# Kernel tuning notes

Hardware: AMD Instinct MI355X
Metric: run time of the kernel (lower is better)

Reference implementation:

```python
import jax, jax.numpy as jnp
import numpy as np

NB_HEAD = 16
SIZE_PER_HEAD = 64
D_MODEL = NB_HEAD * SIZE_PER_HEAD  # 1024
B, L = 2, 2048
NEG_BIG = 1e12


def setup_inputs() -> dict:
    key = jax.random.key(0)
    ks = jax.random.split(key, 8)
    return {
        "Q_seq": jax.random.normal(ks[0], (B, L, D_MODEL), dtype=jnp.float32),
        "K_seq": jax.random.normal(ks[1], (B, L, D_MODEL), dtype=jnp.float32),
        "V_seq": jax.random.normal(ks[2], (B, L, D_MODEL), dtype=jnp.float32),
        "q_len": jax.random.randint(ks[3], (B, 1), 1, L, dtype=jnp.int32),
        "v_len": jax.random.randint(ks[4], (B, 1), 1, L, dtype=jnp.int32),
        "WQ": jax.random.normal(ks[5], (D_MODEL, D_MODEL), dtype=jnp.float32) * 0.02,
        "WK": jax.random.normal(ks[6], (D_MODEL, D_MODEL), dtype=jnp.float32) * 0.02,
        "WV": jax.random.normal(ks[7], (D_MODEL, D_MODEL), dtype=jnp.float32) * 0.02,
    }


def _len_mask(lens, length, dtype):
    # Keras code: mask = 1 - cumsum(one_hot(len, L)) -> 1 for pos < len, 0 otherwise
    return (jnp.arange(length)[None, :] < lens).astype(dtype)  # [B, L]


def reference(Q_seq, K_seq, V_seq, q_len, v_len, WQ, WK, WV):
    Bq, Lq, _ = Q_seq.shape
    Lk = K_seq.shape[1]
    # QKV projections, split heads: [B, H, L, D]
    q = (Q_seq @ WQ).reshape(Bq, Lq, NB_HEAD, SIZE_PER_HEAD).transpose(0, 2, 1, 3)
    k = (K_seq @ WK).reshape(Bq, Lk, NB_HEAD, SIZE_PER_HEAD).transpose(0, 2, 1, 3)
    v = (V_seq @ WV).reshape(Bq, Lk, NB_HEAD, SIZE_PER_HEAD).transpose(0, 2, 1, 3)
    # scaled dot-product scores [B, H, Lq, Lk]
    scores = jnp.einsum("bhqd,bhkd->bhqk", q, k) / np.float32(SIZE_PER_HEAD ** 0.5)
    # additive key-length mask (V_len), matching Mask(..., 'add')
    kmask = _len_mask(v_len, Lk, scores.dtype)  # [B, Lk]
    scores = scores - (1.0 - kmask)[:, None, None, :] * np.float32(NEG_BIG)
    A = jax.nn.softmax(scores, axis=-1)
    # attention output, merge heads: [B, Lq, H*D]
    O = jnp.einsum("bhqk,bhkd->bqhd", A, v).reshape(Bq, Lq, D_MODEL)
    # multiplicative query-length mask (Q_len), matching Mask(..., 'mul')
    qmask = _len_mask(q_len, Lq, O.dtype)  # [B, Lq]
    return O * qmask[:, :, None]
```

## Files before the change

kernel.cpp:

```cpp
#include <hip/hip_runtime.h>
#include <cstddef>

#define NB_HEAD 16
#define HEAD_DIM 64
#define D_MODEL 1024
#define BATCH 2
#define SEQ 2048
#define MROWS (BATCH * SEQ)
#define NSPLIT 2

typedef __bf16 bf16x8 __attribute__((ext_vector_type(8)));
typedef __bf16 bf16x4 __attribute__((ext_vector_type(4)));
typedef float  f32x4  __attribute__((ext_vector_type(4)));

#define XEL ((size_t)MROWS * D_MODEL)
#define WEL ((size_t)D_MODEL * D_MODEL)

static __device__ __forceinline__ size_t xchunk(int row, int k) {
    return ((size_t)(row >> 4) * 32 + (k >> 5)) * 512 + ((k >> 3) & 3) * 128 + (row & 15) * 8 + (k & 7);
}
static __device__ __forceinline__ size_t qkbase(int bh, int row16, int dc) {
    return ((size_t)(bh * 128 + row16) * 2 + dc) * 512;
}
static __device__ __forceinline__ size_t qkelem(int bh, int row, int d) {
    return qkbase(bh, row >> 4, d >> 5) + ((d >> 3) & 3) * 128 + (row & 15) * 8 + (d & 7);
}
static __device__ __forceinline__ size_t vbase(int bh, int d16, int kc) {
    return ((size_t)(bh * 4 + d16) * 64 + kc) * 512;
}
static __device__ __forceinline__ size_t velem(int bh, int d, int key) {
    return vbase(bh, d >> 4, key >> 5) + ((key >> 3) & 3) * 128 + (d & 15) * 8 + (key & 7);
}

static __device__ __forceinline__ void split_bf16(float x, __bf16& h, __bf16& l) {
    h = (__bf16)x;
    l = (__bf16)(x - (float)h);
}

static __device__ __forceinline__ void gload_lds16(const __bf16* g, __bf16* l) {
    __builtin_amdgcn_global_load_lds((const __attribute__((address_space(1))) void*)g,
                                     (__attribute__((address_space(3))) void*)l,
                                     16, 0, 0);
}

__global__ __launch_bounds__(256) void conv_wt_kernel(
    const float* __restrict__ W0, const float* __restrict__ W1,
    const float* __restrict__ W2,
    __bf16* __restrict__ hi, __bf16* __restrict__ lo)
{
    __shared__ float tile[64][65];
    const int t  = threadIdx.x;
    const int k0 = blockIdx.x * 64;
    const int n0 = blockIdx.y * 64;
    const int z  = blockIdx.z;
    const float* W = (z == 0) ? W0 : ((z == 1) ? W1 : W2);
    __bf16* hz = hi + (size_t)z * WEL;
    __bf16* lz = lo + (size_t)z * WEL;

    #pragma unroll
    for (int p = 0; p < 4; ++p) {
        const int e = (p * 256 + t) * 4;
        const int r = e >> 6, c = e & 63;
        const float4 v = *(const float4*)(W + (size_t)(k0 + r) * D_MODEL + n0 + c);
        tile[r][c] = v.x; tile[r][c + 1] = v.y; tile[r][c + 2] = v.z; tile[r][c + 3] = v.w;
    }
    __syncthreads();
    #pragma unroll
    for (int p = 0; p < 4; ++p) {
        const int e = (p * 256 + t) * 4;
        const int n = e >> 6, kc = e & 63;
        __bf16 h[4], l[4];
        #pragma unroll
        for (int u = 0; u < 4; ++u) split_bf16(tile[kc + u][n], h[u], l[u]);
        const size_t a = xchunk(n0 + n, k0 + kc);
        *(bf16x4*)(hz + a) = (bf16x4){h[0], h[1], h[2], h[3]};
        *(bf16x4*)(lz + a) = (bf16x4){l[0], l[1], l[2], l[3]};
    }
}

__global__ __launch_bounds__(256) void conv_x_kernel(
    const float* __restrict__ X0, const float* __restrict__ X1,
    const float* __restrict__ X2,
    const int* __restrict__ q_len, const int* __restrict__ v_len,
    __bf16* __restrict__ xhi, __bf16* __restrict__ xlo)
{
    const int z = blockIdx.y;
    const size_t e = ((size_t)blockIdx.x * 256 + threadIdx.x) * 8;
    const int l = (int)(e >> 10), k = (int)(e & 1023);
    const int bb = l >> 11, lb = l & (SEQ - 1);
    const int len = (z == 0) ? q_len[bb] : v_len[bb];
    if (lb >= ((len + 127) & ~127)) return;

    const float* X = (z == 0) ? X0 : ((z == 1) ? X1 : X2);
    const float4 v0 = *(const float4*)(X + e);
    const float4 v1 = *(const float4*)(X + e + 4);
    const float xs[8] = {v0.x, v0.y, v0.z, v0.w, v1.x, v1.y, v1.z, v1.w};
    bf16x8 h8, l8;
    #pragma unroll
    for (int u = 0; u < 8; ++u) { __bf16 h_, l_; split_bf16(xs[u], h_, l_); h8[u] = h_; l8[u] = l_; }
    const size_t a = z * XEL + xchunk(l, k);
    *(bf16x8*)(xhi + a) = h8;
    *(bf16x8*)(xlo + a) = l8;
}

__global__ __launch_bounds__(256, 3) void proj_mfma_kernel(
    const __bf16* __restrict__ Xhi, const __bf16* __restrict__ Xlo,
    const __bf16* __restrict__ Wchi, const __bf16* __restrict__ Wclo,
    const int* __restrict__ q_len, const int* __restrict__ v_len,
    __bf16* __restrict__ qch, __bf16* __restrict__ qcl,
    __bf16* __restrict__ kch, __bf16* __restrict__ kcl,
    __bf16* __restrict__ vch, __bf16* __restrict__ vcl)
{
    __shared__ __align__(16) __bf16 lds[2][24][512];

    const int t    = threadIdx.x;
    const int wave = t >> 6, lane = t & 63;
    const int li   = lane & 15, grp = lane >> 4;
    const int wm   = wave >> 1, wn = wave & 1;
    const int m0   = blockIdx.x * 128;
    const int n0   = blockIdx.y * 64;
    const int z    = blockIdx.z;
    const int bb   = m0 >> 11;
    const int l0   = m0 & (SEQ - 1);
    const int need = (z == 0) ? q_len[bb] : v_len[bb];
    if (l0 >= need) return;

    const __bf16* Xh = Xhi + z * XEL;
    const __bf16* Xl = Xlo + z * XEL;
    const __bf16* Wh = Wchi + z * WEL;
    const __bf16* Wl = Wclo + z * WEL;

    const __bf16* gs[6];
    #pragma unroll
    for (int u = 0; u < 6; ++u) {
        const int c = u * 4 + wave;
        const __bf16* src;
        int idx;
        if (c < 8)       { src = Xh; idx = (m0 >> 4) + c; }
        else if (c < 16) { src = Xl; idx = (m0 >> 4) + (c - 8); }
        else if (c < 20) { src = Wh; idx = (n0 >> 4) + (c - 16); }
        else             { src = Wl; idx = (n0 >> 4) + (c - 20); }
        gs[u] = src + (size_t)idx * 32 * 512 + (size_t)lane * 8;
    }

    auto STAGE = [&](int buf, int kc) {
        #pragma unroll
        for (int u = 0; u < 6; ++u)
            gload_lds16(gs[u] + (size_t)kc * 512, &lds[buf][u * 4 + wave][0]);
    };

    f32x4 acc[4][2] = {};

    STAGE(0, 0);
    __syncthreads();

    #pragma unroll 2
    for (int kc = 0; kc < 32; ++kc) {
        const int cur = kc & 1;
        if (kc < 31) STAGE(cur ^ 1, kc + 1);

        bf16x8 ah[4], al4[4], bh2[2], bl2[2];
        #pragma unroll
        for (int i = 0; i < 4; ++i) {
            ah[i]  = *(const bf16x8*)&lds[cur][(wm << 2) + i][lane * 8];
            al4[i] = *(const bf16x8*)&lds[cur][8 + (wm << 2) + i][lane * 8];
        }
        #pragma unroll
        for (int j = 0; j < 2; ++j) {
            bh2[j] = *(const bf16x8*)&lds[cur][16 + (wn << 1) + j][lane * 8];
            bl2[j] = *(const bf16x8*)&lds[cur][20 + (wn << 1) + j][lane * 8];
        }
        #pragma unroll
        for (int j = 0; j < 2; ++j) {
            #pragma unroll
            for (int i = 0; i < 4; ++i) {
                acc[i][j] = __builtin_amdgcn_mfma_f32_16x16x32_bf16(ah[i],  bh2[j], acc[i][j], 0, 0, 0);
                acc[i][j] = __builtin_amdgcn_mfma_f32_16x16x32_bf16(ah[i],  bl2[j], acc[i][j], 0, 0, 0);
                acc[i][j] = __builtin_amdgcn_mfma_f32_16x16x32_bf16(al4[i], bh2[j], acc[i][j], 0, 0, 0);
            }
        }
        __syncthreads();
    }

    #pragma unroll
    for (int j = 0; j < 2; ++j) {
        const int cg = n0 + wn * 32 + j * 16 + li;
        const int hd = cg >> 6, d = cg & 63;
        const int bhI = bb * NB_HEAD + hd;
        #pragma unroll
        for (int i = 0; i < 4; ++i) {
            #pragma unroll
            for (int r = 0; r < 4; ++r) {
                const int rg = m0 + wm * 64 + i * 16 + grp * 4 + r;
                const int lg = rg & (SEQ - 1);
                __bf16 h_, l_;
                split_bf16(acc[i][j][r], h_, l_);
                if (z == 0) {
                    const size_t a = qkelem(bhI, lg, d);
                    qch[a] = h_; qcl[a] = l_;
                } else if (z == 1) {
                    const size_t a = qkelem(bhI, lg, d);
                    kch[a] = h_; kcl[a] = l_;
                } else {
                    const size_t a = velem(bhI, d, lg);
                    vch[a] = h_; vcl[a] = l_;
                }
            }
        }
    }
}

__global__ __launch_bounds__(256, 2) void attn_mfma_kernel(
    const __bf16* __restrict__ qch, const __bf16* __restrict__ qcl,
    const __bf16* __restrict__ kch, const __bf16* __restrict__ kcl,
    const __bf16* __restrict__ vch, const __bf16* __restrict__ vcl,
    const int* __restrict__ q_len, const int* __restrict__ v_len,
    float* __restrict__ Opart, float* __restrict__ Mbuf, float* __restrict__ Lbuf)
{
    __shared__ __align__(16) __bf16 Ps[128][72];

    const int t = threadIdx.x;
    const int wq = t >> 6, lane = t & 63;
    const int grp = lane >> 4, li = lane & 15;
    const int hh = blockIdx.x;
    const int split = blockIdx.y & (NSPLIT - 1);
    const int q0 = (blockIdx.y >> 1) * 128;
    const int b  = blockIdx.z;
    const int qlen = q_len[b], vlen = v_len[b];
    const int bh = b * NB_HEAD + hh;
    const int qbase = q0 + wq * 32;

    if (qbase >= qlen) return;

    bf16x8 qh[2][2], ql[2][2];
    #pragma unroll
    for (int s = 0; s < 2; ++s)
        #pragma unroll
        for (int ks = 0; ks < 2; ++ks) {
            const size_t a = qkbase(bh, (qbase >> 4) + s, ks) + lane * 8;
            qh[s][ks] = *(const bf16x8*)(qch + a);
            ql[s][ks] = *(const bf16x8*)(qcl + a);
        }

    f32x4 O[2][4] = {};
    float m_s[2][4], l_s[2][4];
    #pragma unroll
    for (int s = 0; s < 2; ++s)
        #pragma unroll
        for (int r = 0; r < 4; ++r) { m_s[s][r] = -1e30f; l_s[s][r] = 0.f; }

    const int nktT = (vlen + 63) >> 6;
    const int half = (nktT + NSPLIT - 1) / NSPLIT;
    const int tBeg = split * half;
    const int tEnd = (nktT < tBeg + half) ? nktT : (tBeg + half);

    for (int tt = tBeg; tt < tEnd; ++tt) {
        const int k0 = tt * 64;

        f32x4 sacc[2][4] = {};
        #pragma unroll
        for (int ks = 0; ks < 2; ++ks) {
            bf16x8 kh_[4], kl_[4];
            #pragma unroll
            for (int j = 0; j < 4; ++j) {
                const size_t a = qkbase(bh, (k0 >> 4) + j, ks) + lane * 8;
                kh_[j] = *(const bf16x8*)(kch + a);
                kl_[j] = *(const bf16x8*)(kcl + a);
            }
            #pragma unroll
            for (int j = 0; j < 4; ++j)
                #pragma unroll
                for (int s = 0; s < 2; ++s) {
                    sacc[s][j] = __builtin_amdgcn_mfma_f32_16x16x32_bf16(qh[s][ks], kh_[j], sacc[s][j], 0, 0, 0);
                    sacc[s][j] = __builtin_amdgcn_mfma_f32_16x16x32_bf16(qh[s][ks], kl_[j], sacc[s][j], 0, 0, 0);
                    sacc[s][j] = __builtin_amdgcn_mfma_f32_16x16x32_bf16(ql[s][ks], kh_[j], sacc[s][j], 0, 0, 0);
                }
        }

        bf16x8 vh_[2][4], vl_[2][4];
        #pragma unroll
        for (int ks = 0; ks < 2; ++ks)
            #pragma unroll
            for (int j = 0; j < 4; ++j) {
                const size_t a = vbase(bh, j, (k0 >> 5) + ks) + lane * 8;
                vh_[ks][j] = *(const bf16x8*)(vch + a);
                vl_[ks][j] = *(const bf16x8*)(vcl + a);
            }

        #pragma unroll
        for (int s = 0; s < 2; ++s) {
            float mx[4] = {-1e30f, -1e30f, -1e30f, -1e30f};
            #pragma unroll
            for (int j = 0; j < 4; ++j) {
                const int key = k0 + j * 16 + li;
                #pragma unroll
                for (int r = 0; r < 4; ++r) {
                    float v = sacc[s][j][r] * 0.125f;
                    if (key >= vlen) v = -1e30f;
                    sacc[s][j][r] = v;
                    mx[r] = fmaxf(mx[r], v);
                }
            }
            #pragma unroll
            for (int r = 0; r < 4; ++r) {
                mx[r] = fmaxf(mx[r], __shfl_xor(mx[r], 1));
                mx[r] = fmaxf(mx[r], __shfl_xor(mx[r], 2));
                mx[r] = fmaxf(mx[r], __shfl_xor(mx[r], 4));
                mx[r] = fmaxf(mx[r], __shfl_xor(mx[r], 8));
            }
            float al[4], sum[4];
            #pragma unroll
            for (int r = 0; r < 4; ++r) {
                const float mn = fmaxf(m_s[s][r], mx[r]);
                al[r] = __expf(m_s[s][r] - mn);
                m_s[s][r] = mn;
                sum[r] = 0.f;
            }
            #pragma unroll
            for (int j = 0; j < 4; ++j)
                #pragma unroll
                for (int r = 0; r < 4; ++r) {
                    const float p = __expf(sacc[s][j][r] - m_s[s][r]);
                    const __bf16 pb = (__bf16)p;
                    sum[r] += (float)pb;
                    Ps[wq * 32 + s * 16 + grp * 4 + r][j * 16 + li] = pb;
                }
            #pragma unroll
            for (int r = 0; r < 4; ++r) {
                sum[r] += __shfl_xor(sum[r], 1);
                sum[r] += __shfl_xor(sum[r], 2);
                sum[r] += __shfl_xor(sum[r], 4);
                sum[r] += __shfl_xor(sum[r], 8);
                l_s[s][r] = l_s[s][r] * al[r] + sum[r];
            }
            #pragma unroll
            for (int j = 0; j < 4; ++j)
                #pragma unroll
                for (int r = 0; r < 4; ++r) O[s][j][r] *= al[r];
        }
        asm volatile("s_waitcnt lgkmcnt(0)" ::: "memory");

        #pragma unroll
        for (int ks = 0; ks < 2; ++ks) {
            bf16x8 pa[2];
            #pragma unroll
            for (int s = 0; s < 2; ++s)
                pa[s] = *(const bf16x8*)&Ps[wq * 32 + s * 16 + li][ks * 32 + grp * 8];
            #pragma unroll
            for (int j = 0; j < 4; ++j)
                #pragma unroll
                for (int s = 0; s < 2; ++s) {
                    O[s][j] = __builtin_amdgcn_mfma_f32_16x16x32_bf16(pa[s], vh_[ks][j], O[s][j], 0, 0, 0);
                    O[s][j] = __builtin_amdgcn_mfma_f32_16x16x32_bf16(pa[s], vl_[ks][j], O[s][j], 0, 0, 0);
                }
        }
    }

    const size_t osplit = (size_t)split * MROWS * D_MODEL;
    #pragma unroll
    for (int s = 0; s < 2; ++s)
        #pragma unroll
        for (int r = 0; r < 4; ++r) {
            const int q = qbase + s * 16 + grp * 4 + r;
            if (q < qlen) {
                #pragma unroll
                for (int j = 0; j < 4; ++j)
                    Opart[osplit + ((size_t)b * SEQ + q) * D_MODEL + hh * HEAD_DIM + j * 16 + li] = O[s][j][r];
                if (li == 0) {
                    const size_t mi = (((size_t)split * BATCH + b) * NB_HEAD + hh) * SEQ + q;
                    Mbuf[mi] = m_s[s][r];
                    Lbuf[mi] = l_s[s][r];
                }
            }
        }
}

__global__ __launch_bounds__(256) void attn_merge_kernel(
    const float* __restrict__ Opart, const float* __restrict__ Mbuf,
    const float* __restrict__ Lbuf, const int* __restrict__ q_len,
    float* __restrict__ out)
{
    const int row = blockIdx.x;
    const int b = row >> 11, q = row & (SEQ - 1);
    const int col = threadIdx.x * 4;
    const int hh = col >> 6;
    const size_t oidx = (size_t)row * D_MODEL + col;

    float4 o = make_float4(0.f, 0.f, 0.f, 0.f);
    if (q < q_len[b]) {
        const size_t mlsz = (size_t)BATCH * NB_HEAD * SEQ;
        const size_t mi = ((size_t)b * NB_HEAD + hh) * SEQ + q;
        const float m0 = Mbuf[mi], m1 = Mbuf[mlsz + mi];
        const float l0 = Lbuf[mi], l1 = Lbuf[mlsz + mi];
        const float M  = fmaxf(m0, m1);
        const float w0 = __expf(m0 - M), w1 = __expf(m1 - M);
        const float inv = 1.f / (l0 * w0 + l1 * w1);
        const float4 a = *(const float4*)(Opart + oidx);
        const float4 c = *(const float4*)(Opart + (size_t)MROWS * D_MODEL + oidx);
        o.x = (a.x * w0 + c.x * w1) * inv;
        o.y = (a.y * w0 + c.y * w1) * inv;
        o.z = (a.z * w0 + c.z * w1) * inv;
        o.w = (a.w * w0 + c.w * w1) * inv;
    }
    *(float4*)(out + oidx) = o;
}

extern "C" void kernel_launch(void* const* d_in, const int* in_sizes, int n_in,
                              void* d_out, int out_size, void* d_ws, size_t ws_size,
                              hipStream_t stream)
{
    (void)in_sizes; (void)n_in; (void)out_size; (void)ws_size;
    const float* Q_seq = (const float*)d_in[0];
    const float* K_seq = (const float*)d_in[1];
    const float* V_seq = (const float*)d_in[2];
    const int*   q_len = (const int*)d_in[3];
    const int*   v_len = (const int*)d_in[4];
    const float* WQ    = (const float*)d_in[5];
    const float* WK    = (const float*)d_in[6];
    const float* WV    = (const float*)d_in[7];
    float* out = (float*)d_out;

    __bf16* wchi = (__bf16*)d_ws;
    __bf16* wclo = wchi + 3 * WEL;
    __bf16* xhi_ = wclo + 3 * WEL;
    __bf16* xlo_ = xhi_ + 3 * XEL;
    __bf16* qch_ = xlo_ + 3 * XEL;
    __bf16* qcl_ = qch_ + XEL;
    __bf16* kch_ = qcl_ + XEL;
    __bf16* kcl_ = kch_ + XEL;
    __bf16* vch_ = kcl_ + XEL;
    __bf16* vcl_ = vch_ + XEL;

    float* Opart = (float*)xhi_;
    float* Mbuf  = (float*)wchi;
    float* Lbuf  = Mbuf + (size_t)NSPLIT * BATCH * NB_HEAD * SEQ;

    dim3 blk(256);

    dim3 cg(D_MODEL / 64, D_MODEL / 64, 3);
    conv_wt_kernel<<<cg, blk, 0, stream>>>(WQ, WK, WV, wchi, wclo);

    dim3 xg((unsigned)(XEL / 2048), 3);
    conv_x_kernel<<<xg, blk, 0, stream>>>(Q_seq, K_seq, V_seq, q_len, v_len, xhi_, xlo_);

    dim3 pg(MROWS / 128, D_MODEL / 64, 3);
    proj_mfma_kernel<<<pg, blk, 0, stream>>>(xhi_, xlo_, wchi, wclo, q_len, v_len,
                                             qch_, qcl_, kch_, kcl_, vch_, vcl_);

    dim3 ag(NB_HEAD, (SEQ / 128) * NSPLIT, BATCH);
    attn_mfma_kernel<<<ag, blk, 0, stream>>>(qch_, qcl_, kch_, kcl_, vch_, vcl_,
                                             q_len, v_len, Opart, Mbuf, Lbuf);

    attn_merge_kernel<<<dim3(MROWS), blk, 0, stream>>>(Opart, Mbuf, Lbuf, q_len, out);
}
```

Baseline: 275.2 us.

## Fold softmax scale into Q, use exp2, lazy rescale, MFMA row sums

The 1/sqrt(d)*log2(e) factor is folded into Q when it is written out, so the attention loop can use exp2 without a per-score multiply. Masking is skipped for fully valid key tiles. Rescaling of O and l is deferred unless some row's max grows by more than 8 (FA4-style lazy rescale), and row sums of P come from an MFMA against a ones vector instead of shuffle reductions. This removes VALU, exp and shuffle work in the softmax stage, at the cost of two extra MFMAs per tile and a larger (but bounded) range for P values.

New measurement: 272.5 us. Within noise of the previous version (-1.0%).

```diff
diff --git a/kernel.cpp b/kernel.cpp
--- a/kernel.cpp
+++ b/kernel.cpp
@@ -15,6 +15,8 @@
 
 #define XEL ((size_t)MROWS * D_MODEL)
 #define WEL ((size_t)D_MODEL * D_MODEL)
+
+#define QSCALE 0.18033688011112042f
 
 static __device__ __forceinline__ size_t xchunk(int row, int k) {
     return ((size_t)(row >> 4) * 32 + (k >> 5)) * 512 + ((k >> 3) & 3) * 128 + (row & 15) * 8 + (k & 7);
@@ -194,14 +196,16 @@
                 const int rg = m0 + wm * 64 + i * 16 + grp * 4 + r;
                 const int lg = rg & (SEQ - 1);
                 __bf16 h_, l_;
-                split_bf16(acc[i][j][r], h_, l_);
                 if (z == 0) {
+                    split_bf16(acc[i][j][r] * QSCALE, h_, l_);
                     const size_t a = qkelem(bhI, lg, d);
                     qch[a] = h_; qcl[a] = l_;
                 } else if (z == 1) {
+                    split_bf16(acc[i][j][r], h_, l_);
                     const size_t a = qkelem(bhI, lg, d);
                     kch[a] = h_; kcl[a] = l_;
                 } else {
+                    split_bf16(acc[i][j][r], h_, l_);
                     const size_t a = velem(bhI, d, lg);
                     vch[a] = h_; vcl[a] = l_;
                 }
@@ -232,6 +236,10 @@
 
     if (qbase >= qlen) return;
 
+    bf16x8 onesv;
+    #pragma unroll
+    for (int u = 0; u < 8; ++u) onesv[u] = (__bf16)1.0f;
+
     bf16x8 qh[2][2], ql[2][2];
     #pragma unroll
     for (int s = 0; s < 2; ++s)
@@ -256,6 +264,7 @@
 
     for (int tt = tBeg; tt < tEnd; ++tt) {
         const int k0 = tt * 64;
+        const bool full = (k0 + 64 <= vlen);
 
         f32x4 sacc[2][4] = {};
         #pragma unroll
@@ -287,18 +296,27 @@
                 vl_[ks][j] = *(const bf16x8*)(vcl + a);
             }
 
+        float mxs[2][4];
+        int defer = 1;
         #pragma unroll
         for (int s = 0; s < 2; ++s) {
             float mx[4] = {-1e30f, -1e30f, -1e30f, -1e30f};
-            #pragma unroll
-            for (int j = 0; j < 4; ++j) {
-                const int key = k0 + j * 16 + li;
-                #pragma unroll
-                for (int r = 0; r < 4; ++r) {
-                    float v = sacc[s][j][r] * 0.125f;
-                    if (key >= vlen) v = -1e30f;
-                    sacc[s][j][r] = v;
-                    mx[r] = fmaxf(mx[r], v);
+            if (full) {
+                #pragma unroll
+                for (int j = 0; j < 4; ++j)
+                    #pragma unroll
+                    for (int r = 0; r < 4; ++r) mx[r] = fmaxf(mx[r], sacc[s][j][r]);
+            } else {
+                #pragma unroll
+                for (int j = 0; j < 4; ++j) {
+                    const int key = k0 + j * 16 + li;
+                    #pragma unroll
+                    for (int r = 0; r < 4; ++r) {
+                        float v = sacc[s][j][r];
+                        if (key >= vlen) v = -1e30f;
+                        sacc[s][j][r] = v;
+                        mx[r] = fmaxf(mx[r], v);
+                    }
                 }
             }
             #pragma unroll
@@ -307,53 +325,65 @@
                 mx[r] = fmaxf(mx[r], __shfl_xor(mx[r], 2));
                 mx[r] = fmaxf(mx[r], __shfl_xor(mx[r], 4));
                 mx[r] = fmaxf(mx[r], __shfl_xor(mx[r], 8));
-            }
-            float al[4], sum[4];
-            #pragma unroll
-            for (int r = 0; r < 4; ++r) {
-                const float mn = fmaxf(m_s[s][r], mx[r]);
-                al[r] = __expf(m_s[s][r] - mn);
-                m_s[s][r] = mn;
-                sum[r] = 0.f;
-            }
+                mxs[s][r] = mx[r];
+                defer &= (mx[r] - m_s[s][r] <= 8.f) ? 1 : 0;
+            }
+        }
+
+        if (!__all(defer)) {
+            #pragma unroll
+            for (int s = 0; s < 2; ++s) {
+                float al[4];
+                #pragma unroll
+                for (int r = 0; r < 4; ++r) {
+                    const float mn = fmaxf(m_s[s][r], mxs[s][r]);
+                    al[r] = exp2f(m_s[s][r] - mn);
+                    m_s[s][r] = mn;
+                    l_s[s][r] *= al[r];
+                }
+                #pragma unroll
+                for (int j = 0; j < 4; ++j)
+                    #pragma unroll
+                    for (int r = 0; r < 4; ++r) O[s][j][r] *= al[r];
+            }
+        }
+
+        #pragma unroll
+        for (int s = 0; s < 2; ++s)
             #pragma unroll
             for (int j = 0; j < 4; ++j)
                 #pragma unroll
                 for (int r = 0; r < 4; ++r) {
-                    const float p = __expf(sacc[s][j][r] - m_s[s][r]);
-                    const __bf16 pb = (__bf16)p;
-                    sum[r] += (float)pb;
-                    Ps[wq * 32 + s * 16 + grp * 4 + r][j * 16 + li] = pb;
-                }
-            #pragma unroll
-            for (int r = 0; r < 4; ++r) {
-                sum[r] += __shfl_xor(sum[r], 1);
-                sum[r] += __shfl_xor(sum[r], 2);
-                sum[r] += __shfl_xor(sum[r], 4);
-                sum[r] += __shfl_xor(sum[r], 8);
-                l_s[s][r] = l_s[s][r] * al[r] + sum[r];
-            }
+                    const float p = exp2f(sacc[s][j][r] - m_s[s][r]);
+                    Ps[wq * 32 + s * 16 + grp * 4 + r][j * 16 + li] = (__bf16)p;
+                }
+        asm volatile("s_waitcnt lgkmcnt(0)" ::: "memory");
+
+        bf16x8 pa[2][2];
+        #pragma unroll
+        for (int s = 0; s < 2; ++s)
+            #pragma unroll
+            for (int ks = 0; ks < 2; ++ks)
+                pa[s][ks] = *(const bf16x8*)&Ps[wq * 32 + s * 16 + li][ks * 32 + grp * 8];
+
+        #pragma unroll
+        for (int s = 0; s < 2; ++s) {
+            f32x4 lsum = {};
+            lsum = __builtin_amdgcn_mfma_f32_16x16x32_bf16(pa[s][0], onesv, lsum, 0, 0, 0);
+            lsum = __builtin_amdgcn_mfma_f32_16x16x32_bf16(pa[s][1], onesv, lsum, 0, 0, 0);
+            #pragma unroll
+            for (int r = 0; r < 4; ++r) l_s[s][r] += lsum[r];
+        }
+
+        #pragma unroll
+        for (int ks = 0; ks < 2; ++ks)
             #pragma unroll
             for (int j = 0; j < 4; ++j)
                 #pragma unroll
-                for (int r = 0; r < 4; ++r) O[s][j][r] *= al[r];
-        }
-        asm volatile("s_waitcnt lgkmcnt(0)" ::: "memory");
-
-        #pragma unroll
-        for (int ks = 0; ks < 2; ++ks) {
-            bf16x8 pa[2];
-            #pragma unroll
-            for (int s = 0; s < 2; ++s)
-                pa[s] = *(const bf16x8*)&Ps[wq * 32 + s * 16 + li][ks * 32 + grp * 8];
-            #pragma unroll
-            for (int j = 0; j < 4; ++j)
-                #pragma unroll
                 for (int s = 0; s < 2; ++s) {
-                    O[s][j] = __builtin_amdgcn_mfma_f32_16x16x32_bf16(pa[s], vh_[ks][j], O[s][j], 0, 0, 0);
-                    O[s][j] = __builtin_amdgcn_mfma_f32_16x16x32_bf16(pa[s], vl_[ks][j], O[s][j], 0, 0, 0);
-                }
-        }
+                    O[s][j] = __builtin_amdgcn_mfma_f32_16x16x32_bf16(pa[s][ks], vh_[ks][j], O[s][j], 0, 0, 0);
+                    O[s][j] = __builtin_amdgcn_mfma_f32_16x16x32_bf16(pa[s][ks], vl_[ks][j], O[s][j], 0, 0, 0);
+                }
     }
 
     const size_t osplit = (size_t)split * MROWS * D_MODEL;
@@ -393,7 +423,7 @@
         const float m0 = Mbuf[mi], m1 = Mbuf[mlsz + mi];
         const float l0 = Lbuf[mi], l1 = Lbuf[mlsz + mi];
         const float M  = fmaxf(m0, m1);
-        const float w0 = __expf(m0 - M), w1 = __expf(m1 - M);
+        const float w0 = exp2f(m0 - M), w1 = exp2f(m1 - M);
         const float inv = 1.f / (l0 * w0 + l1 * w1);
         const float4 a = *(const float4*)(Opart + oidx);
         const float4 c = *(const float4*)(Opart + (size_t)MROWS * D_MODEL + oidx);
```
